# Optimization experiments

Hardware: AMD Instinct MI355X
Metric: run time of the kernel (lower is better)

Reference implementation:

```python
import jax, jax.numpy as jnp
import numpy as np

D_MODEL = 1024
NUM_HEADS = 16
D_K = D_MODEL // NUM_HEADS
B, S = 2, 2048


def setup_inputs() -> dict:
    key = jax.random.key(0)
    ks = jax.random.split(key, 6)
    scale = 1.0 / np.sqrt(D_MODEL)
    x = jax.random.normal(ks[0], (B, S, D_MODEL), dtype=jnp.float32)
    # causal mask: 1 where masked (future positions), per masked_fill(mask == 1, -inf)
    mask = jnp.triu(jnp.ones((S, S), dtype=jnp.int32), k=1)
    Wq = jax.random.normal(ks[1], (D_MODEL, D_MODEL), dtype=jnp.float32) * scale
    Wk = jax.random.normal(ks[2], (D_MODEL, D_MODEL), dtype=jnp.float32) * scale
    Wv = jax.random.normal(ks[3], (D_MODEL, D_MODEL), dtype=jnp.float32) * scale
    Wo = jax.random.normal(ks[4], (D_MODEL, D_MODEL), dtype=jnp.float32) * scale
    zeros = jnp.zeros((D_MODEL,), dtype=jnp.float32)
    return {"x": x, "mask": mask, "Wq": Wq, "bq": zeros, "Wk": Wk, "bk": zeros,
            "Wv": Wv, "bv": zeros, "Wo": Wo, "bo": zeros}


def reference(x, mask, Wq, bq, Wk, bk, Wv, bv, Wo, bo):
    b, s, d = x.shape
    # linear projections (torch nn.Linear: x @ W^T + b; here W stored as [in, out])
    Q = x @ Wq + bq
    K = x @ Wk + bk
    V = x @ Wv + bv
    # split heads -> (b, h, s, d_k)
    def split(t):
        return t.reshape(b, s, NUM_HEADS, D_K).transpose(0, 2, 1, 3)
    Q, K, V = split(Q), split(K), split(V)
    scale = 1.0 / jnp.sqrt(jnp.float32(D_K))
    scores = jnp.einsum("bhqd,bhkd->bhqk", Q, K) * scale  # (b,h,s,s)
    scores = jnp.where(mask[None, None, :, :] == 1, -jnp.inf, scores)
    attn = jax.nn.softmax(scores, axis=-1)
    out = jnp.einsum("bhqk,bhkd->bhqd", attn, V)
    out = out.transpose(0, 2, 1, 3).reshape(b, s, d)  # concat heads
    return out @ Wo + bo
```

## Files before the change

### kernel.cpp

```cpp
#include <hip/hip_runtime.h>
#include <hip/hip_bf16.h>
#include <cstdint>
#include <cmath>

#define DM 1024
#define NH 16
#define DK 64
#define NB 2
#define SS 2048
#define MM (NB*SS)

typedef unsigned short u16;
typedef uint32_t u32;
typedef __attribute__((ext_vector_type(4))) float f32x4;
typedef __attribute__((ext_vector_type(8))) short s16x8;
typedef __attribute__((ext_vector_type(2))) uint32_t u32x2;

__device__ __forceinline__ u16 f2bf(float f) {
    __hip_bfloat16 h = __float2bfloat16(f);
    return __builtin_bit_cast(u16, h);
}
__device__ __forceinline__ float bf2f(u16 u) {
    u32 x = (u32)u << 16;
    return __builtin_bit_cast(float, x);
}

__device__ __forceinline__ u32 cvtpk(float a, float b) {
    u32 r;
    asm("v_cvt_pk_bf16_f32 %0, %1, %2" : "=v"(r) : "v"(a), "v"(b));
    return r;
}

__device__ __forceinline__ void gload_lds16(void* lds, const void* g) {
    __builtin_amdgcn_global_load_lds(
        (const __attribute__((address_space(1))) uint32_t*)g,
        (__attribute__((address_space(3))) uint32_t*)lds, 16, 0, 0);
}

__device__ __forceinline__ int swz(int row, int cb) {
    return row * 128 + ((((cb) >> 4) ^ (row & 7)) << 4) + ((cb) & 15);
}

__global__ void mha_prep(const float* __restrict__ x, u16* __restrict__ xb,
                         const float* __restrict__ W0, const float* __restrict__ W1,
                         const float* __restrict__ W2, const float* __restrict__ W3,
                         u16* __restrict__ WtBase) {
    const int bid = blockIdx.x, tid = threadIdx.x;
    if (bid < 4096) {
        int i = (bid * 256 + tid) * 4;
        float4 v = *reinterpret_cast<const float4*>(x + i);
        ushort4 o;
        o.x = f2bf(v.x); o.y = f2bf(v.y); o.z = f2bf(v.z); o.w = f2bf(v.w);
        *reinterpret_cast<ushort4*>(xb + i) = o;
        return;
    }
    __shared__ float t[32][33];
    const int b2 = bid - 4096;
    const int mat = b2 >> 10, rem = b2 & 1023;
    const int cx = rem & 31, cy = rem >> 5;
    const float* W = (mat == 0) ? W0 : (mat == 1) ? W1 : (mat == 2) ? W2 : W3;
    u16* Wt = WtBase + (size_t)mat * DM * DM;
    const int c0 = cx * 32, r0 = cy * 32;
    const int tx = tid & 31, ty = tid >> 5;
#pragma unroll
    for (int i = ty; i < 32; i += 8)
        t[i][tx] = W[(size_t)(r0 + i) * DM + c0 + tx];
    __syncthreads();
#pragma unroll
    for (int i = ty; i < 32; i += 8)
        Wt[(size_t)(c0 + i) * DM + r0 + tx] = f2bf(t[tx][i]);
}

__device__ __forceinline__ void gemm_loop(const u16* __restrict__ A, const u16* __restrict__ Bt,
                                          int m0, int n0,
                                          u16 (*As)[64], u16 (*Bs)[64], f32x4 acc[4][4]) {
    const int tid = threadIdx.x;
    const int wave = tid >> 6, lane = tid & 63;
    const int lr = lane & 15, kg = lane >> 4;
    const int wr = wave >> 1, wc = wave & 1;

    for (int k0 = 0; k0 < DM; k0 += 64) {
        __syncthreads();
#pragma unroll
        for (int i = 0; i < 4; ++i) {
            const int o   = ((wave * 4 + i) * 64 + lane) * 16;
            const int row = o >> 7;
            const int kb  = o & 127;
            gload_lds16((char*)As + o, A  + (size_t)(m0 + row) * DM + k0 + (kb >> 1));
            gload_lds16((char*)Bs + o, Bt + (size_t)(n0 + row) * DM + k0 + (kb >> 1));
        }
        __syncthreads();
#pragma unroll
        for (int kk = 0; kk < 64; kk += 32) {
            s16x8 a[4], b[4];
#pragma unroll
            for (int m = 0; m < 4; ++m)
                a[m] = *reinterpret_cast<const s16x8*>(&As[wr * 64 + m * 16 + lr][kk + kg * 8]);
#pragma unroll
            for (int n = 0; n < 4; ++n)
                b[n] = *reinterpret_cast<const s16x8*>(&Bs[wc * 64 + n * 16 + lr][kk + kg * 8]);
#pragma unroll
            for (int m = 0; m < 4; ++m)
#pragma unroll
                for (int n = 0; n < 4; ++n)
                    acc[m][n] = __builtin_amdgcn_mfma_f32_16x16x32_bf16(a[m], b[n], acc[m][n], 0, 0, 0);
        }
    }
}

__global__ __launch_bounds__(256, 2) void mha_gemm_qkv(const u16* __restrict__ xb, const u16* __restrict__ Wt,
                                                       const float* __restrict__ bq, const float* __restrict__ bk,
                                                       const float* __restrict__ bv, u16* __restrict__ qkv) {
    __shared__ __align__(16) char smem[32768];
    u16 (*As)[64] = reinterpret_cast<u16(*)[64]>(smem);
    u16 (*Bs)[64] = reinterpret_cast<u16(*)[64]>(smem + 16384);

    const int bid = blockIdx.x;
    const int j = bid & 7, r = bid >> 3;
    const int bx = j * 4 + (r & 3);
    const int by = (r >> 2) & 7;
    const int z  = r >> 5;
    const int m0 = bx * 128, n0 = by * 128;

    const float* bias = (z == 0) ? bq : (z == 1) ? bk : bv;
    const float scale = (z == 0) ? 0.125f * 1.44269504088896f : 1.0f;
    u16* Cout = qkv + (size_t)z * MM * DM;

    f32x4 acc[4][4] = {};
    gemm_loop(xb, Wt + (size_t)z * DM * DM, m0, n0, As, Bs, acc);

    const int tid = threadIdx.x;
    const int wave = tid >> 6, lane = tid & 63;
    const int lr = lane & 15, kg = lane >> 4;
    const int wr = wave >> 1, wc = wave & 1;

    __syncthreads();
#pragma unroll
    for (int m = 0; m < 4; ++m)
#pragma unroll
        for (int n = 0; n < 4; ++n) {
            const int col = wc * 64 + n * 16 + lr;
            const float bv2 = bias[n0 + col];
#pragma unroll
            for (int j2 = 0; j2 < 4; ++j2) {
                const int row = wr * 64 + m * 16 + kg * 4 + j2;
                const float v = (acc[m][n][j2] + bv2) * scale;
                int imgoff;
                if (z == 0) {
                    imgoff = row * 256 + (col >> 6) * 128 + (col & 63) * 2;
                } else if (z == 1) {
                    imgoff = ((row >> 6) * 2 + (col >> 6)) * 8192 + swz(row & 63, (col & 63) * 2);
                } else {
                    imgoff = ((row >> 6) * 2 + (col >> 6)) * 8192
                           + swz(col & 63, ((row & 63) >> 1) * 4 + (row & 1) * 2);
                }
                *reinterpret_cast<u16*>(smem + imgoff) = f2bf(v);
            }
        }
    __syncthreads();
    const int bb = m0 >> 11, s0 = m0 & (SS - 1);
    const int kt0 = s0 >> 6, h0 = n0 >> 6;
#pragma unroll
    for (int it = 0; it < 8; ++it) {
        const int c = it * 256 + tid;
        const s16x8 v = *reinterpret_cast<const s16x8*>(smem + c * 16);
        u16* dst;
        if (z == 0) {
            const int srow = c >> 4, inrow = c & 15;
            const int hl = inrow >> 3, d0 = (inrow & 7) * 8;
            dst = Cout + (((size_t)(bb * NH + h0 + hl) * SS + (s0 + srow)) * DK) + d0;
        } else {
            const int quad = c >> 9, off = (c & 511) * 8;
            const int ktl = quad >> 1, hl = quad & 1;
            dst = Cout + ((size_t)(bb * NH + h0 + hl) * 32 + kt0 + ktl) * 4096 + off;
        }
        *reinterpret_cast<s16x8*>(dst) = v;
    }
}

__global__ __launch_bounds__(256, 2) void mha_gemm_out(const u16* __restrict__ AO, const u16* __restrict__ WoT,
                                                       const float* __restrict__ bo, float* __restrict__ out) {
    __shared__ __align__(16) char smem[32768];
    u16 (*As)[64] = reinterpret_cast<u16(*)[64]>(smem);
    u16 (*Bs)[64] = reinterpret_cast<u16(*)[64]>(smem + 16384);

    const int bid = blockIdx.x;
    const int j = bid & 7, r = bid >> 3;
    const int bx = j * 4 + (r & 3);
    const int by = r >> 2;
    const int m0 = bx * 128, n0 = by * 128;

    f32x4 acc[4][4] = {};
    gemm_loop(AO, WoT, m0, n0, As, Bs, acc);

    const int tid = threadIdx.x;
    const int wave = tid >> 6, lane = tid & 63;
    const int lr = lane & 15, kg = lane >> 4;
    const int wr = wave >> 1, wc = wave & 1;
#pragma unroll
    for (int m = 0; m < 4; ++m)
#pragma unroll
        for (int n = 0; n < 4; ++n) {
            const int col = n0 + wc * 64 + n * 16 + lr;
            const float bv = bo[col];
#pragma unroll
            for (int j2 = 0; j2 < 4; ++j2) {
                const int row = m0 + wr * 64 + m * 16 + kg * 4 + j2;
                out[(size_t)row * DM + col] = acc[m][n][j2] + bv;
            }
        }
}

__device__ const unsigned char JQT[48] = {
    15,31,30,31, 14,29,30,28,29, 13,27,28,26,27, 12,25,26,24,25,
    11,23,24,22,23, 10,21,22,20,21, 9,19,20,18,19, 8,17,18,16,17,
    7,16, 6,5,4,3,2,1,0};
__device__ const unsigned char JKS[48] = {
    0,0,15,16, 0,0,0,14,15, 0,0,0,13,14, 0,0,0,12,13,
    0,0,0,11,12, 0,0,0,10,11, 0,0,0,9,10, 0,0,0,8,9,
    0,0, 0,0,0,0,0,0,0};
__device__ const unsigned char JKL[48] = {
    16,16,16,16, 15,15,15,15,15, 14,14,14,14,14, 13,13,13,13,13,
    12,12,12,12,12, 11,11,11,11,11, 10,10,10,10,10, 9,9,9,9,9,
    8,8, 7,6,5,4,3,2,1};
__device__ const unsigned char JSL[48] = {
    255,30,29,31, 255,26,28,25,27, 255,22,24,21,23, 255,18,20,17,19,
    255,14,16,13,15, 255,10,12,9,11, 255,6,8,5,7, 255,2,4,1,3,
    255,0, 255,255,255,255,255,255,255};

__global__ __launch_bounds__(256, 4) void mha_attn(const u16* __restrict__ Qb, const u16* __restrict__ Kswz,
                                                   const u16* __restrict__ Vtswz, u16* __restrict__ AO,
                                                   u16* __restrict__ Opart, float* __restrict__ lpart) {
    __shared__ __align__(16) char lds[40960];

    const int bid = blockIdx.x;
    const int bh  = bid & 31;
    const int job = bid >> 5;
    const int qt   = JQT[job];
    const int kst  = JKS[job];
    const int klen = JKL[job];
    const int slot = JSL[job];
    const int qb = qt * 64;

    const int tid = threadIdx.x, w = tid >> 6, lane = tid & 63;
    const int lr = lane & 15, kg = lane >> 4;

    const u16* Qh = Qb + (size_t)bh * SS * DK;
    const char* Ktiles = (const char*)(Kswz  + (size_t)bh * 32 * 4096);
    const char* Vtiles = (const char*)(Vtswz + (size_t)bh * 32 * 4096);
    const int bb = bh >> 4, hh = bh & (NH - 1);
    char* psb = lds + 32768 + w * 2048;
    const int o = tid * 16;

    const int qrow = qb + w * 16 + lr;
    const s16x8 qf0 = *reinterpret_cast<const s16x8*>(Qh + (size_t)qrow * DK + kg * 8);
    const s16x8 qf1 = *reinterpret_cast<const s16x8*>(Qh + (size_t)qrow * DK + 32 + kg * 8);
    f32x4 accO[4] = {};
    float lp = 0.f;

    const int kend = kst + klen;
    {
        const char* Kt = Ktiles + kst * 8192;
        const char* Vt = Vtiles + kst * 8192;
        gload_lds16(lds + o,                 Kt + o);
        gload_lds16(lds + o + 4096,          Kt + o + 4096);
        gload_lds16(lds + 16384 + o,         Vt + o);
        gload_lds16(lds + 16384 + o + 4096,  Vt + o + 4096);
    }

    for (int t = kst; t < kend; ++t) {
        const int buf = (t - kst) & 1;
        asm volatile("s_waitcnt vmcnt(0)" ::: "memory");
        __syncthreads();
        if (t + 1 < kend) {
            const char* Kt = Ktiles + (t + 1) * 8192;
            const char* Vt = Vtiles + (t + 1) * 8192;
            char* kb2 = lds + (buf ^ 1) * 8192;
            char* vb2 = lds + 16384 + (buf ^ 1) * 8192;
            gload_lds16(kb2 + o,        Kt + o);
            gload_lds16(kb2 + o + 4096, Kt + o + 4096);
            gload_lds16(vb2 + o,        Vt + o);
            gload_lds16(vb2 + o + 4096, Vt + o + 4096);
        }
        const char* ksb = lds + buf * 8192;
        const char* vtb = lds + 16384 + buf * 8192;

        f32x4 sc[4];
#pragma unroll
        for (int f = 0; f < 4; ++f) {
            s16x8 kf0 = *reinterpret_cast<const s16x8*>(ksb + swz(f * 16 + lr, kg * 16));
            s16x8 kf1 = *reinterpret_cast<const s16x8*>(ksb + swz(f * 16 + lr, 64 + kg * 16));
            f32x4 s = {};
            s = __builtin_amdgcn_mfma_f32_16x16x32_bf16(kf0, qf0, s, 0, 0, 0);
            s = __builtin_amdgcn_mfma_f32_16x16x32_bf16(kf1, qf1, s, 0, 0, 0);
            sc[f] = s;
        }
#pragma unroll
        for (int f = 0; f < 4; ++f)
#pragma unroll
            for (int j = 0; j < 4; ++j)
                sc[f][j] = __builtin_amdgcn_exp2f(sc[f][j]);
        if (t == qt) {
            const int qloc = w * 16 + lr;
#pragma unroll
            for (int f = 0; f < 4; ++f) {
                const int kc = f * 16 + kg * 4;
#pragma unroll
                for (int j = 0; j < 4; ++j)
                    if (kc + j > qloc) sc[f][j] = 0.f;
            }
        }
        float fs0 = 0.f, fs1 = 0.f;
#pragma unroll
        for (int f = 0; f < 4; ++f) {
            u32x2 pp;
            pp[0] = cvtpk(sc[f][0], sc[f][1]);
            pp[1] = cvtpk(sc[f][2], sc[f][3]);
            *reinterpret_cast<u32x2*>(psb + swz(lr, f * 32 + kg * 8)) = pp;
            const float s01 = sc[f][0] + sc[f][1], s23 = sc[f][2] + sc[f][3];
            if (f & 1) fs1 += s01 + s23; else fs0 += s01 + s23;
        }
        lp += fs0 + fs1;

        const s16x8 pf0 = *reinterpret_cast<const s16x8*>(psb + swz(lr, kg * 16));
        const s16x8 pf1 = *reinterpret_cast<const s16x8*>(psb + swz(lr, 64 + kg * 16));
#pragma unroll
        for (int db = 0; db < 4; ++db) {
            s16x8 vf0 = *reinterpret_cast<const s16x8*>(vtb + swz(db * 16 + lr, kg * 16));
            s16x8 vf1 = *reinterpret_cast<const s16x8*>(vtb + swz(db * 16 + lr, 64 + kg * 16));
            accO[db] = __builtin_amdgcn_mfma_f32_16x16x32_bf16(pf0, vf0, accO[db], 0, 0, 0);
            accO[db] = __builtin_amdgcn_mfma_f32_16x16x32_bf16(pf1, vf1, accO[db], 0, 0, 0);
        }
    }

    lp += __shfl_xor(lp, 16, 64);
    lp += __shfl_xor(lp, 32, 64);

    if (slot == 255) {
        float inv[4];
#pragma unroll
        for (int j = 0; j < 4; ++j)
            inv[j] = 1.0f / __shfl(lp, kg * 4 + j, 64);
#pragma unroll
        for (int db = 0; db < 4; ++db) {
            const int d = db * 16 + lr;
#pragma unroll
            for (int j = 0; j < 4; ++j) {
                const int s = qb + w * 16 + kg * 4 + j;
                AO[((size_t)(bb * SS + s)) * DM + hh * DK + d] = f2bf(accO[db][j] * inv[j]);
            }
        }
    } else {
        const int idx = bh * 32 + slot;
        u16* Od = Opart + (size_t)idx * 4096;
#pragma unroll
        for (int db = 0; db < 4; ++db) {
            const int d = db * 16 + lr;
#pragma unroll
            for (int j = 0; j < 4; ++j)
                Od[(w * 16 + kg * 4 + j) * 64 + d] = f2bf(accO[db][j]);
        }
        if (lane < 16)
            lpart[idx * 64 + w * 16 + lane] = lp;
    }
}

__global__ __launch_bounds__(256) void mha_combine(const u16* __restrict__ Opart,
                                                   const float* __restrict__ lpart,
                                                   u16* __restrict__ AO) {
    const int blk = blockIdx.x;
    const int bh = blk & 31, q = blk >> 5;
    const int qt = 16 + q;
    const int t = threadIdx.x;
    const int row = t >> 2, c0 = (t & 3) * 16;
    const int idx0 = bh * 32 + q * 2;
    const u16* O0 = Opart + (size_t)idx0 * 4096 + row * 64 + c0;
    const u16* O1 = O0 + 4096;
    const float l = lpart[idx0 * 64 + row] + lpart[(idx0 + 1) * 64 + row];
    const float inv = 1.0f / l;
    const int bb = bh >> 4, hh = bh & (NH - 1);
    const int s = qt * 64 + row;
    u16* dst = AO + ((size_t)(bb * SS + s)) * DM + hh * DK + c0;
#pragma unroll
    for (int h = 0; h < 2; ++h) {
        s16x8 a = *reinterpret_cast<const s16x8*>(O0 + h * 8);
        s16x8 b = *reinterpret_cast<const s16x8*>(O1 + h * 8);
        u16* ap = (u16*)&a; u16* bp = (u16*)&b;
        u16 ov[8];
#pragma unroll
        for (int i = 0; i < 8; ++i)
            ov[i] = f2bf((bf2f(ap[i]) + bf2f(bp[i])) * inv);
        *reinterpret_cast<ushort4*>(dst + h * 8) = *reinterpret_cast<ushort4*>(&ov[0]);
        *reinterpret_cast<ushort4*>(dst + h * 8 + 4) = *reinterpret_cast<ushort4*>(&ov[4]);
    }
}

extern "C" void kernel_launch(void* const* d_in, const int* in_sizes, int n_in,
                              void* d_out, int out_size, void* d_ws, size_t ws_size,
                              hipStream_t stream) {
    const float* x  = (const float*)d_in[0];
    const float* Wq = (const float*)d_in[2];
    const float* bq = (const float*)d_in[3];
    const float* Wk = (const float*)d_in[4];
    const float* bk = (const float*)d_in[5];
    const float* Wv = (const float*)d_in[6];
    const float* bv = (const float*)d_in[7];
    const float* Wo = (const float*)d_in[8];
    const float* bo = (const float*)d_in[9];
    float* out = (float*)d_out;

    char* ws = (char*)d_ws;
    u16* xb  = (u16*)(ws);
    u16* Wt  = (u16*)(ws + ((size_t)8  << 20));
    u16* qkv = (u16*)(ws + ((size_t)16 << 20));
    u16* AO  = (u16*)(ws + ((size_t)40 << 20));
    u16*   Opart = (u16*)(ws);
    float* lpart = (float*)(ws + ((size_t)8 << 20));

    mha_prep<<<dim3(8192), dim3(256), 0, stream>>>(x, xb, Wq, Wk, Wv, Wo, Wt);
    mha_gemm_qkv<<<dim3(768), dim3(256), 0, stream>>>(xb, Wt, bq, bk, bv, qkv);
    mha_attn<<<dim3(1536), dim3(256), 0, stream>>>(qkv, qkv + (size_t)4194304, qkv + (size_t)8388608,
                                                   AO, Opart, lpart);
    mha_combine<<<dim3(512), dim3(256), 0, stream>>>(Opart, lpart, AO);
    mha_gemm_out<<<dim3(256), dim3(256), 0, stream>>>(AO, Wt + (size_t)3 * DM * DM, bo, out);
}
```

Measured before the change: 109.0 us.

## Double-buffer LDS in GEMM main loop and simplify block indexing

Replaces the single-buffered GEMM K-loop with a two-stage LDS double buffer: the next K-tile is issued via direct global-to-LDS loads before computing on the current one, and partial vmcnt waits plus explicit barriers stand in for the two __syncthreads. LDS per block doubles to 64KB, which may limit blocks per CU. Block indexing drops the grouped swizzle in favour of a plain 3D/2D grid, which may hurt L2 locality.

```diff
diff --git a/kernel.cpp b/kernel.cpp
--- a/kernel.cpp
+++ b/kernel.cpp
@@ -71,25 +71,40 @@
         Wt[(size_t)(c0 + i) * DM + r0 + tx] = f2bf(t[tx][i]);
 }
 
-__device__ __forceinline__ void gemm_loop(const u16* __restrict__ A, const u16* __restrict__ Bt,
-                                          int m0, int n0,
-                                          u16 (*As)[64], u16 (*Bs)[64], f32x4 acc[4][4]) {
+__device__ __forceinline__ void gemm_loop_db(const u16* __restrict__ A, const u16* __restrict__ Bt,
+                                             int m0, int n0, char* smem , f32x4 acc[4][4]) {
     const int tid = threadIdx.x;
     const int wave = tid >> 6, lane = tid & 63;
     const int lr = lane & 15, kg = lane >> 4;
     const int wr = wave >> 1, wc = wave & 1;
 
-    for (int k0 = 0; k0 < DM; k0 += 64) {
-        __syncthreads();
+    auto STAGE = [&](int buf, int k0) {
+        char* As = smem + buf * 32768;
+        char* Bs = As + 16384;
 #pragma unroll
         for (int i = 0; i < 4; ++i) {
             const int o   = ((wave * 4 + i) * 64 + lane) * 16;
             const int row = o >> 7;
             const int kb  = o & 127;
-            gload_lds16((char*)As + o, A  + (size_t)(m0 + row) * DM + k0 + (kb >> 1));
-            gload_lds16((char*)Bs + o, Bt + (size_t)(n0 + row) * DM + k0 + (kb >> 1));
-        }
-        __syncthreads();
+            gload_lds16(As + o, A  + (size_t)(m0 + row) * DM + k0 + (kb >> 1));
+            gload_lds16(Bs + o, Bt + (size_t)(n0 + row) * DM + k0 + (kb >> 1));
+        }
+    };
+
+    STAGE(0, 0);
+    for (int t = 0; t < 16; ++t) {
+        if (t + 1 < 16) {
+            STAGE((t + 1) & 1, (t + 1) * 64);
+            asm volatile("s_waitcnt vmcnt(8)" ::: "memory");
+        } else {
+            asm volatile("s_waitcnt vmcnt(0)" ::: "memory");
+        }
+        __builtin_amdgcn_sched_barrier(0);
+        __builtin_amdgcn_s_barrier();
+        __builtin_amdgcn_sched_barrier(0);
+
+        const u16 (*As)[64] = reinterpret_cast<const u16(*)[64]>(smem + (t & 1) * 32768);
+        const u16 (*Bs)[64] = reinterpret_cast<const u16(*)[64]>(smem + (t & 1) * 32768 + 16384);
 #pragma unroll
         for (int kk = 0; kk < 64; kk += 32) {
             s16x8 a[4], b[4];
@@ -105,36 +120,30 @@
                 for (int n = 0; n < 4; ++n)
                     acc[m][n] = __builtin_amdgcn_mfma_f32_16x16x32_bf16(a[m], b[n], acc[m][n], 0, 0, 0);
         }
+        __builtin_amdgcn_sched_barrier(0);
+        __builtin_amdgcn_s_barrier();
+        __builtin_amdgcn_sched_barrier(0);
     }
 }
 
 __global__ __launch_bounds__(256, 2) void mha_gemm_qkv(const u16* __restrict__ xb, const u16* __restrict__ Wt,
                                                        const float* __restrict__ bq, const float* __restrict__ bk,
                                                        const float* __restrict__ bv, u16* __restrict__ qkv) {
-    __shared__ __align__(16) char smem[32768];
-    u16 (*As)[64] = reinterpret_cast<u16(*)[64]>(smem);
-    u16 (*Bs)[64] = reinterpret_cast<u16(*)[64]>(smem + 16384);
-
-    const int bid = blockIdx.x;
-    const int j = bid & 7, r = bid >> 3;
-    const int bx = j * 4 + (r & 3);
-    const int by = (r >> 2) & 7;
-    const int z  = r >> 5;
-    const int m0 = bx * 128, n0 = by * 128;
-
+    __shared__ __align__(16) char smem[65536];
+    const int m0 = blockIdx.x * 128, n0 = blockIdx.y * 128;
+    const int z = blockIdx.z;
     const float* bias = (z == 0) ? bq : (z == 1) ? bk : bv;
     const float scale = (z == 0) ? 0.125f * 1.44269504088896f : 1.0f;
     u16* Cout = qkv + (size_t)z * MM * DM;
 
     f32x4 acc[4][4] = {};
-    gemm_loop(xb, Wt + (size_t)z * DM * DM, m0, n0, As, Bs, acc);
+    gemm_loop_db(xb, Wt + (size_t)z * DM * DM, m0, n0, smem, acc);
 
     const int tid = threadIdx.x;
     const int wave = tid >> 6, lane = tid & 63;
     const int lr = lane & 15, kg = lane >> 4;
     const int wr = wave >> 1, wc = wave & 1;
 
-    __syncthreads();
 #pragma unroll
     for (int m = 0; m < 4; ++m)
 #pragma unroll
@@ -180,18 +189,11 @@
 
 __global__ __launch_bounds__(256, 2) void mha_gemm_out(const u16* __restrict__ AO, const u16* __restrict__ WoT,
                                                        const float* __restrict__ bo, float* __restrict__ out) {
-    __shared__ __align__(16) char smem[32768];
-    u16 (*As)[64] = reinterpret_cast<u16(*)[64]>(smem);
-    u16 (*Bs)[64] = reinterpret_cast<u16(*)[64]>(smem + 16384);
-
-    const int bid = blockIdx.x;
-    const int j = bid & 7, r = bid >> 3;
-    const int bx = j * 4 + (r & 3);
-    const int by = r >> 2;
-    const int m0 = bx * 128, n0 = by * 128;
+    __shared__ __align__(16) char smem[65536];
+    const int m0 = blockIdx.x * 128, n0 = blockIdx.y * 128;
 
     f32x4 acc[4][4] = {};
-    gemm_loop(AO, WoT, m0, n0, As, Bs, acc);
+    gemm_loop_db(AO, WoT, m0, n0, smem, acc);
 
     const int tid = threadIdx.x;
     const int wave = tid >> 6, lane = tid & 63;
@@ -418,9 +420,9 @@
     float* lpart = (float*)(ws + ((size_t)8 << 20));
 
     mha_prep<<<dim3(8192), dim3(256), 0, stream>>>(x, xb, Wq, Wk, Wv, Wo, Wt);
-    mha_gemm_qkv<<<dim3(768), dim3(256), 0, stream>>>(xb, Wt, bq, bk, bv, qkv);
+    mha_gemm_qkv<<<dim3(32, 8, 3), dim3(256), 0, stream>>>(xb, Wt, bq, bk, bv, qkv);
     mha_attn<<<dim3(1536), dim3(256), 0, stream>>>(qkv, qkv + (size_t)4194304, qkv + (size_t)8388608,
                                                    AO, Opart, lpart);
     mha_combine<<<dim3(512), dim3(256), 0, stream>>>(Opart, lpart, AO);
-    mha_gemm_out<<<dim3(256), dim3(256), 0, stream>>>(AO, Wt + (size_t)3 * DM * DM, bo, out);
-}
+    mha_gemm_out<<<dim3(32, 8), dim3(256), 0, stream>>>(AO, Wt + (size_t)3 * DM * DM, bo, out);
+}
```

New measurement: 107.3 us. Within noise of the previous version (-1.6%).
